# Optimization experiments

Measured on AMD Instinct MI355X. Metric: run time of the kernel, lower is better.

Reference implementation:

```python
import jax, jax.numpy as jnp
import numpy as np

NUM_GROUPS = 256   # number of distinct gt instance ids per image
EPS = 1e-6
PULL_W = 1.0
PUSH_W = 1.0
LOSS_W = 1.0


def setup_inputs() -> dict:
    key = jax.random.key(0)
    k1, k2, k3 = jax.random.split(key, 3)
    B, N, D = 16, 16384, 256
    pred = jax.random.normal(k1, (B, N, D), dtype=jnp.float32)
    gt_inds = jax.random.randint(k2, (B, N), 0, NUM_GROUPS, dtype=jnp.int32)
    anchor_inds = jax.random.randint(k3, (B, N), 0, 9, dtype=jnp.int32)
    return {"pred": pred, "gt_inds": gt_inds, "anchor_inds": anchor_inds}


def _single_image_loss(p, g):
    # p: [N, D] tag embeddings, g: [N] int group ids in [0, NUM_GROUPS)
    ones = jnp.ones(g.shape, dtype=p.dtype)
    counts = jax.ops.segment_sum(ones, g, num_segments=NUM_GROUPS)          # [G]
    sums = jax.ops.segment_sum(p, g, num_segments=NUM_GROUPS)               # [G, D]
    tags = sums / jnp.maximum(counts, 1.0)[:, None]                         # group means

    # pull: per-element cosine to own group's tag (torch cos eps clamp on norm product)
    tag_per = tags[g]                                                       # [N, D]
    dot = jnp.sum(p * tag_per, axis=1)
    denom = jnp.maximum(jnp.linalg.norm(p, axis=1) * jnp.linalg.norm(tag_per, axis=1), EPS)
    one_minus_cos = 1.0 - dot / denom                                       # [N]
    pull_g = jax.ops.segment_sum(one_minus_cos, g, num_segments=NUM_GROUPS) / jnp.maximum(counts, 1.0)

    present = counts > 0
    obj_num = jnp.sum(present.astype(p.dtype))
    pull = jnp.sum(jnp.where(present, pull_g, 0.0)) / (obj_num + EPS)

    # push: pairwise cosine over group tags (incl. diagonal, then subtract 2*obj_num)
    tn = jnp.linalg.norm(tags, axis=1)                                      # [G]
    cosmat = (tags @ tags.T) / jnp.maximum(tn[:, None] * tn[None, :], EPS)  # [G, G]
    pair_mask = present[:, None] & present[None, :]
    push_sum = jnp.sum(jnp.where(pair_mask, 1.0 + cosmat, 0.0)) - 2.0 * obj_num
    push = push_sum / (((obj_num - 1.0) * obj_num + EPS) * 2.0)

    loss = PUSH_W * push + PULL_W * pull
    # original returns 0 when only a single group exists
    return jnp.where(obj_num > 1.0, loss, 0.0)


def reference(pred, gt_inds, anchor_inds):
    per_img = jax.vmap(_single_image_loss)(pred, gt_inds)   # [B]
    return LOSS_W * jnp.mean(per_img)
```

## Files before the change

### kernel.cpp

```cpp
#include <hip/hip_runtime.h>

#define B_ 16
#define N_ 16384
#define D_ 256
#define G_ 256
#define EPSF 1e-6f
#define CHUNKS 16
#define CROWS (N_/CHUNKS)

template <int CTRL>
__device__ __forceinline__ float dpp_add_step(float x) {
    const int y = __builtin_amdgcn_update_dpp(0, __float_as_int(x), CTRL, 0xF, 0xF, false);
    return x + __int_as_float(y);
}
__device__ __forceinline__ float wave_sum64(float x) {
    x = dpp_add_step<0x111>(x);
    x = dpp_add_step<0x112>(x);
    x = dpp_add_step<0x114>(x);
    x = dpp_add_step<0x118>(x);
    x = dpp_add_step<0x142>(x);
    x = dpp_add_step<0x143>(x);
    return __int_as_float(__builtin_amdgcn_readlane(__float_as_int(x), 63));
}

__global__ __launch_bounds__(256) void k_hist(const int* __restrict__ gt,
                                              int* __restrict__ chist,
                                              int* __restrict__ done) {
    __shared__ int h[G_];
    const int tid = threadIdx.x, blk = blockIdx.x;
    if (blk == 0 && tid == 0) done[0] = 0;
    h[tid] = 0;
    __syncthreads();
    const int4 g4 = *(const int4*)&gt[blk*CROWS + tid*4];
    atomicAdd(&h[g4.x], 1);
    atomicAdd(&h[g4.y], 1);
    atomicAdd(&h[g4.z], 1);
    atomicAdd(&h[g4.w], 1);
    __syncthreads();
    chist[blk*G_ + tid] = h[tid];
}

__global__ __launch_bounds__(256) void k_scatscan(const int* __restrict__ gt,
                                                  const int* __restrict__ chist,
                                                  int* __restrict__ counts,
                                                  int* __restrict__ starts,
                                                  int* __restrict__ sorted) {
    __shared__ int scn[G_];
    __shared__ int cur[G_];
    const int g = threadIdx.x, blk = blockIdx.x;
    const int b = blk >> 4, chunk = blk & 15;

    int tot = 0, pre = 0;
    #pragma unroll
    for (int cc = 0; cc < CHUNKS; ++cc) {
        const int v = chist[((b<<4) + cc)*G_ + g];
        pre += (cc < chunk) ? v : 0;
        tot += v;
    }
    scn[g] = tot;
    __syncthreads();
    for (int off = 1; off < G_; off <<= 1) {
        const int v2 = (g >= off) ? scn[g - off] : 0;
        __syncthreads();
        scn[g] += v2;
        __syncthreads();
    }
    const int st = scn[g] - tot;
    if (chunk == 0) { counts[b*G_ + g] = tot; starts[b*G_ + g] = st; }
    cur[g] = st + pre;
    __syncthreads();

    const int rbase = chunk * CROWS;
    const int4 g4 = *(const int4*)&gt[b*N_ + rbase + g*4];
    const int r = rbase + g*4;
    int* sb = sorted + b*N_;
    sb[atomicAdd(&cur[g4.x], 1)] = r;
    sb[atomicAdd(&cur[g4.y], 1)] = r + 1;
    sb[atomicAdd(&cur[g4.z], 1)] = r + 2;
    sb[atomicAdd(&cur[g4.w], 1)] = r + 3;
}

__global__ __launch_bounds__(256, 5) void k_fused(const float* __restrict__ pred,
                                                  const int* __restrict__ sorted,
                                                  const int* __restrict__ starts,
                                                  const int* __restrict__ counts,
                                                  float* __restrict__ sums,
                                                  float* __restrict__ pull_g) {
    __shared__ float comb[2][2][2][D_];
    const int tid = threadIdx.x, lane = tid & 63, w = tid >> 6;
    const int sub = w >> 1, h = w & 1;
    const int gi = (blockIdx.x << 1) | sub;
    const int b = gi >> 8;
    const int start = starts[gi], cnt = counts[gi];
    const int c = lane * 4;

    const float* predb = pred + (size_t)b*N_*D_;
    const int*   sortb = sorted + b*N_ + start;

    float4 acc  = make_float4(0.f,0.f,0.f,0.f);
    float4 uacc = make_float4(0.f,0.f,0.f,0.f);

    const int half = (cnt + 1) >> 1;
    const int lo = h * half;
    const int hi = min(cnt, lo + half);
    int i = lo;

    if (cnt > 0 && cnt <= 128) {
        const int ids0 = sortb[min(lane, cnt-1)];
        int ids1 = 0;
        if (cnt > 64) ids1 = sortb[min(64 + lane, cnt-1)];
        #define GET2(k) (((k) < 64) ? __builtin_amdgcn_readlane(ids0, (k)) \
                                    : __builtin_amdgcn_readlane(ids1, (k) - 64))
        for (; i + 8 <= hi; i += 8) {
            const int r0 = GET2(i+0), r1 = GET2(i+1), r2 = GET2(i+2), r3 = GET2(i+3);
            const int r4 = GET2(i+4), r5 = GET2(i+5), r6 = GET2(i+6), r7 = GET2(i+7);
            const float4 p0 = *(const float4*)&predb[(size_t)r0*D_ + c];
            const float4 p1 = *(const float4*)&predb[(size_t)r1*D_ + c];
            const float4 p2 = *(const float4*)&predb[(size_t)r2*D_ + c];
            const float4 p3 = *(const float4*)&predb[(size_t)r3*D_ + c];
            const float4 p4 = *(const float4*)&predb[(size_t)r4*D_ + c];
            const float4 p5 = *(const float4*)&predb[(size_t)r5*D_ + c];
            const float4 p6 = *(const float4*)&predb[(size_t)r6*D_ + c];
            const float4 p7 = *(const float4*)&predb[(size_t)r7*D_ + c];
            float n0 = p0.x*p0.x + p0.y*p0.y + p0.z*p0.z + p0.w*p0.w;
            float n1 = p1.x*p1.x + p1.y*p1.y + p1.z*p1.z + p1.w*p1.w;
            float n2 = p2.x*p2.x + p2.y*p2.y + p2.z*p2.z + p2.w*p2.w;
            float n3 = p3.x*p3.x + p3.y*p3.y + p3.z*p3.z + p3.w*p3.w;
            float n4 = p4.x*p4.x + p4.y*p4.y + p4.z*p4.z + p4.w*p4.w;
            float n5 = p5.x*p5.x + p5.y*p5.y + p5.z*p5.z + p5.w*p5.w;
            float n6 = p6.x*p6.x + p6.y*p6.y + p6.z*p6.z + p6.w*p6.w;
            float n7 = p7.x*p7.x + p7.y*p7.y + p7.z*p7.z + p7.w*p7.w;
            n0 = wave_sum64(n0); n1 = wave_sum64(n1);
            n2 = wave_sum64(n2); n3 = wave_sum64(n3);
            n4 = wave_sum64(n4); n5 = wave_sum64(n5);
            n6 = wave_sum64(n6); n7 = wave_sum64(n7);
            const float q0 = __frsqrt_rn(n0), q1 = __frsqrt_rn(n1);
            const float q2 = __frsqrt_rn(n2), q3 = __frsqrt_rn(n3);
            const float q4 = __frsqrt_rn(n4), q5 = __frsqrt_rn(n5);
            const float q6 = __frsqrt_rn(n6), q7 = __frsqrt_rn(n7);
            acc.x  += ((p0.x + p1.x) + (p2.x + p3.x)) + ((p4.x + p5.x) + (p6.x + p7.x));
            acc.y  += ((p0.y + p1.y) + (p2.y + p3.y)) + ((p4.y + p5.y) + (p6.y + p7.y));
            acc.z  += ((p0.z + p1.z) + (p2.z + p3.z)) + ((p4.z + p5.z) + (p6.z + p7.z));
            acc.w  += ((p0.w + p1.w) + (p2.w + p3.w)) + ((p4.w + p5.w) + (p6.w + p7.w));
            uacc.x += ((p0.x*q0 + p1.x*q1) + (p2.x*q2 + p3.x*q3)) + ((p4.x*q4 + p5.x*q5) + (p6.x*q6 + p7.x*q7));
            uacc.y += ((p0.y*q0 + p1.y*q1) + (p2.y*q2 + p3.y*q3)) + ((p4.y*q4 + p5.y*q5) + (p6.y*q6 + p7.y*q7));
            uacc.z += ((p0.z*q0 + p1.z*q1) + (p2.z*q2 + p3.z*q3)) + ((p4.z*q4 + p5.z*q5) + (p6.z*q6 + p7.z*q7));
            uacc.w += ((p0.w*q0 + p1.w*q1) + (p2.w*q2 + p3.w*q3)) + ((p4.w*q4 + p5.w*q5) + (p6.w*q6 + p7.w*q7));
        }
        for (; i < hi; ++i) {
            const int r0 = GET2(i);
            const float4 p0 = *(const float4*)&predb[(size_t)r0*D_ + c];
            const float n0 = wave_sum64(p0.x*p0.x + p0.y*p0.y + p0.z*p0.z + p0.w*p0.w);
            const float q0 = __frsqrt_rn(n0);
            acc.x  += p0.x;    acc.y  += p0.y;    acc.z  += p0.z;    acc.w  += p0.w;
            uacc.x += p0.x*q0; uacc.y += p0.y*q0; uacc.z += p0.z*q0; uacc.w += p0.w*q0;
        }
        #undef GET2
    } else if (cnt > 128) {
        for (; i < hi; ++i) {
            const int r0 = sortb[i];
            const float4 p0 = *(const float4*)&predb[(size_t)r0*D_ + c];
            const float n0 = wave_sum64(p0.x*p0.x + p0.y*p0.y + p0.z*p0.z + p0.w*p0.w);
            const float q0 = __frsqrt_rn(n0);
            acc.x  += p0.x;    acc.y  += p0.y;    acc.z  += p0.z;    acc.w  += p0.w;
            uacc.x += p0.x*q0; uacc.y += p0.y*q0; uacc.z += p0.z*q0; uacc.w += p0.w*q0;
        }
    }

    *(float4*)&comb[sub][h][0][c] = acc;
    *(float4*)&comb[sub][h][1][c] = uacc;
    __syncthreads();
    if (h != 0) return;

    const float4 a2 = *(const float4*)&comb[sub][1][0][c];
    const float4 u2 = *(const float4*)&comb[sub][1][1][c];
    acc.x  += a2.x;  acc.y  += a2.y;  acc.z  += a2.z;  acc.w  += a2.w;
    uacc.x += u2.x;  uacc.y += u2.y;  uacc.z += u2.z;  uacc.w += u2.w;

    *(float4*)&sums[(size_t)gi*D_ + c] = acc;
    if (cnt == 0) {
        if (lane == 0) pull_g[gi] = 0.f;
        return;
    }
    const float ssq = wave_sum64(acc.x*acc.x + acc.y*acc.y + acc.z*acc.z + acc.w*acc.w);
    const float dus = wave_sum64(uacc.x*acc.x + uacc.y*acc.y + uacc.z*acc.z + uacc.w*acc.w);
    if (lane == 0) pull_g[gi] = (float)cnt - dus / sqrtf(ssq);
}

__global__ __launch_bounds__(256) void k_tags(const float* __restrict__ sums,
                                              const int* __restrict__ counts,
                                              const float* __restrict__ pull_g,
                                              float* __restrict__ lossv,
                                              int* __restrict__ done,
                                              float* __restrict__ out) {
    const int b = blockIdx.x;
    const int tid = threadIdx.x;
    const int lane = tid & 63;
    const int wave = tid >> 6;
    __shared__ float s_acc[D_];
    __shared__ float redA[256];
    __shared__ float redB[256];

    for (int i = tid; i < D_; i += 256) s_acc[i] = 0.f;
    __syncthreads();

    const int c = lane * 4;
    float4 sl = make_float4(0.f, 0.f, 0.f, 0.f);
    for (int g = wave; g < G_; g += 4) {
        const int cnt = counts[b*G_ + g];
        const float inv = 1.0f / fmaxf((float)cnt, 1.0f);
        const float4 sm = *(const float4*)&sums[((size_t)(b*G_ + g))*D_ + c];
        const float tx = sm.x*inv, tyv = sm.y*inv, tz = sm.z*inv, tw = sm.w*inv;
        const float sq = wave_sum64(tx*tx + tyv*tyv + tz*tz + tw*tw);
        if (cnt > 0) {
            const float it = __frsqrt_rn(sq);
            sl.x += tx*it; sl.y += tyv*it; sl.z += tz*it; sl.w += tw*it;
        }
    }
    atomicAdd(&s_acc[c+0], sl.x);
    atomicAdd(&s_acc[c+1], sl.y);
    atomicAdd(&s_acc[c+2], sl.z);
    atomicAdd(&s_acc[c+3], sl.w);
    __syncthreads();

    const int cnt_t = counts[b*G_ + tid];
    const float v = s_acc[tid];
    redA[tid] = v * v;
    redB[tid] = (cnt_t > 0) ? 1.f : 0.f;
    __syncthreads();
    for (int s = 128; s > 0; s >>= 1) {
        if (tid < s) { redA[tid] += redA[tid + s]; redB[tid] += redB[tid + s]; }
        __syncthreads();
    }
    float ssq = 0.f, obj = 0.f;
    if (tid == 0) { ssq = redA[0]; obj = redB[0]; }
    __syncthreads();

    redA[tid] = (cnt_t > 0) ? pull_g[b*G_ + tid] / (float)cnt_t : 0.f;
    __syncthreads();
    for (int s = 128; s > 0; s >>= 1) {
        if (tid < s) redA[tid] += redA[tid + s];
        __syncthreads();
    }
    if (tid == 0) {
        const float push = (obj*obj - 2.f*obj + ssq) / (((obj - 1.f)*obj + EPSF) * 2.f);
        const float pull = redA[0] / (obj + EPSF);
        const float loss = (obj > 1.f) ? (push + pull) : 0.f;
        __hip_atomic_store(&lossv[b], loss, __ATOMIC_RELEASE, __HIP_MEMORY_SCOPE_AGENT);
        const int o = __hip_atomic_fetch_add(&done[0], 1, __ATOMIC_ACQ_REL,
                                             __HIP_MEMORY_SCOPE_AGENT);
        if (o == B_ - 1) {
            float t = 0.f;
            #pragma unroll
            for (int bb = 0; bb < B_; ++bb)
                t += __hip_atomic_load(&lossv[bb], __ATOMIC_RELAXED, __HIP_MEMORY_SCOPE_AGENT);
            out[0] = t * (1.0f / (float)B_);
        }
    }
}

extern "C" void kernel_launch(void* const* d_in, const int* in_sizes, int n_in,
                              void* d_out, int out_size, void* d_ws, size_t ws_size,
                              hipStream_t stream) {
    const float* pred = (const float*)d_in[0];
    const int*   gt   = (const int*)d_in[1];
    float* out = (float*)d_out;

    char* ws = (char*)d_ws;
    const size_t SZ_SUMS = (size_t)B_*G_*D_*sizeof(float);
    const size_t SZ_I    = (size_t)B_*G_*sizeof(int);

    float* sums    = (float*)ws;                               ws += SZ_SUMS;
    int*   counts  = (int*)ws;                                 ws += SZ_I;
    int*   starts  = (int*)ws;                                 ws += SZ_I;
    float* pull_g  = (float*)ws;                               ws += SZ_I;
    float* lossv   = (float*)ws;                               ws += 64*sizeof(float);
    int*   done    = (int*)ws;                                 ws += 64*sizeof(int);
    int*   sorted  = (int*)ws;                                 ws += (size_t)B_*N_*sizeof(int);
    int*   chist   = (int*)ws;

    k_hist     <<<B_*CHUNKS, 256, 0, stream>>>(gt, chist, done);
    k_scatscan <<<B_*CHUNKS, 256, 0, stream>>>(gt, chist, counts, starts, sorted);
    k_fused    <<<B_*G_/2,   256, 0, stream>>>(pred, sorted, starts, counts, sums, pull_g);
    k_tags     <<<B_,        256, 0, stream>>>(sums, counts, pull_g, lossv, done, out);
}
```

Baseline: 85.44 us.

## Map one wave per group and unroll gather loop by sixteen with masking

Each wave now handles a whole group instead of two waves splitting a group and combining through shared memory with a block barrier. The grid shrinks to four groups per block. The small-group path becomes a 16-way unrolled loop with clamped indices and zero weights for the tail, so more loads are in flight per wave. Empty groups exit early. In exchange each wave carries twice the serial work, the tail iterations issue redundant loads, and the heavier register use comes with a lower occupancy hint.

```diff
diff --git a/kernel.cpp b/kernel.cpp
--- a/kernel.cpp
+++ b/kernel.cpp
@@ -80,84 +80,61 @@
     sb[atomicAdd(&cur[g4.w], 1)] = r + 3;
 }
 
-__global__ __launch_bounds__(256, 5) void k_fused(const float* __restrict__ pred,
+__global__ __launch_bounds__(256, 4) void k_fused(const float* __restrict__ pred,
                                                   const int* __restrict__ sorted,
                                                   const int* __restrict__ starts,
                                                   const int* __restrict__ counts,
                                                   float* __restrict__ sums,
                                                   float* __restrict__ pull_g) {
-    __shared__ float comb[2][2][2][D_];
     const int tid = threadIdx.x, lane = tid & 63, w = tid >> 6;
-    const int sub = w >> 1, h = w & 1;
-    const int gi = (blockIdx.x << 1) | sub;
+    const int gi = (blockIdx.x << 2) | w;
     const int b = gi >> 8;
     const int start = starts[gi], cnt = counts[gi];
     const int c = lane * 4;
 
+    if (cnt == 0) {
+        float4 z = make_float4(0.f,0.f,0.f,0.f);
+        *(float4*)&sums[(size_t)gi*D_ + c] = z;
+        if (lane == 0) pull_g[gi] = 0.f;
+        return;
+    }
+
     const float* predb = pred + (size_t)b*N_*D_;
     const int*   sortb = sorted + b*N_ + start;
 
     float4 acc  = make_float4(0.f,0.f,0.f,0.f);
     float4 uacc = make_float4(0.f,0.f,0.f,0.f);
 
-    const int half = (cnt + 1) >> 1;
-    const int lo = h * half;
-    const int hi = min(cnt, lo + half);
-    int i = lo;
-
-    if (cnt > 0 && cnt <= 128) {
+    if (cnt <= 128) {
         const int ids0 = sortb[min(lane, cnt-1)];
         int ids1 = 0;
         if (cnt > 64) ids1 = sortb[min(64 + lane, cnt-1)];
-        #define GET2(k) (((k) < 64) ? __builtin_amdgcn_readlane(ids0, (k)) \
-                                    : __builtin_amdgcn_readlane(ids1, (k) - 64))
-        for (; i + 8 <= hi; i += 8) {
-            const int r0 = GET2(i+0), r1 = GET2(i+1), r2 = GET2(i+2), r3 = GET2(i+3);
-            const int r4 = GET2(i+4), r5 = GET2(i+5), r6 = GET2(i+6), r7 = GET2(i+7);
-            const float4 p0 = *(const float4*)&predb[(size_t)r0*D_ + c];
-            const float4 p1 = *(const float4*)&predb[(size_t)r1*D_ + c];
-            const float4 p2 = *(const float4*)&predb[(size_t)r2*D_ + c];
-            const float4 p3 = *(const float4*)&predb[(size_t)r3*D_ + c];
-            const float4 p4 = *(const float4*)&predb[(size_t)r4*D_ + c];
-            const float4 p5 = *(const float4*)&predb[(size_t)r5*D_ + c];
-            const float4 p6 = *(const float4*)&predb[(size_t)r6*D_ + c];
-            const float4 p7 = *(const float4*)&predb[(size_t)r7*D_ + c];
-            float n0 = p0.x*p0.x + p0.y*p0.y + p0.z*p0.z + p0.w*p0.w;
-            float n1 = p1.x*p1.x + p1.y*p1.y + p1.z*p1.z + p1.w*p1.w;
-            float n2 = p2.x*p2.x + p2.y*p2.y + p2.z*p2.z + p2.w*p2.w;
-            float n3 = p3.x*p3.x + p3.y*p3.y + p3.z*p3.z + p3.w*p3.w;
-            float n4 = p4.x*p4.x + p4.y*p4.y + p4.z*p4.z + p4.w*p4.w;
-            float n5 = p5.x*p5.x + p5.y*p5.y + p5.z*p5.z + p5.w*p5.w;
-            float n6 = p6.x*p6.x + p6.y*p6.y + p6.z*p6.z + p6.w*p6.w;
-            float n7 = p7.x*p7.x + p7.y*p7.y + p7.z*p7.z + p7.w*p7.w;
-            n0 = wave_sum64(n0); n1 = wave_sum64(n1);
-            n2 = wave_sum64(n2); n3 = wave_sum64(n3);
-            n4 = wave_sum64(n4); n5 = wave_sum64(n5);
-            n6 = wave_sum64(n6); n7 = wave_sum64(n7);
-            const float q0 = __frsqrt_rn(n0), q1 = __frsqrt_rn(n1);
-            const float q2 = __frsqrt_rn(n2), q3 = __frsqrt_rn(n3);
-            const float q4 = __frsqrt_rn(n4), q5 = __frsqrt_rn(n5);
-            const float q6 = __frsqrt_rn(n6), q7 = __frsqrt_rn(n7);
-            acc.x  += ((p0.x + p1.x) + (p2.x + p3.x)) + ((p4.x + p5.x) + (p6.x + p7.x));
-            acc.y  += ((p0.y + p1.y) + (p2.y + p3.y)) + ((p4.y + p5.y) + (p6.y + p7.y));
-            acc.z  += ((p0.z + p1.z) + (p2.z + p3.z)) + ((p4.z + p5.z) + (p6.z + p7.z));
-            acc.w  += ((p0.w + p1.w) + (p2.w + p3.w)) + ((p4.w + p5.w) + (p6.w + p7.w));
-            uacc.x += ((p0.x*q0 + p1.x*q1) + (p2.x*q2 + p3.x*q3)) + ((p4.x*q4 + p5.x*q5) + (p6.x*q6 + p7.x*q7));
-            uacc.y += ((p0.y*q0 + p1.y*q1) + (p2.y*q2 + p3.y*q3)) + ((p4.y*q4 + p5.y*q5) + (p6.y*q6 + p7.y*q7));
-            uacc.z += ((p0.z*q0 + p1.z*q1) + (p2.z*q2 + p3.z*q3)) + ((p4.z*q4 + p5.z*q5) + (p6.z*q6 + p7.z*q7));
-            uacc.w += ((p0.w*q0 + p1.w*q1) + (p2.w*q2 + p3.w*q3)) + ((p4.w*q4 + p5.w*q5) + (p6.w*q6 + p7.w*q7));
-        }
-        for (; i < hi; ++i) {
-            const int r0 = GET2(i);
-            const float4 p0 = *(const float4*)&predb[(size_t)r0*D_ + c];
-            const float n0 = wave_sum64(p0.x*p0.x + p0.y*p0.y + p0.z*p0.z + p0.w*p0.w);
-            const float q0 = __frsqrt_rn(n0);
-            acc.x  += p0.x;    acc.y  += p0.y;    acc.z  += p0.z;    acc.w  += p0.w;
-            uacc.x += p0.x*q0; uacc.y += p0.y*q0; uacc.z += p0.z*q0; uacc.w += p0.w*q0;
-        }
-        #undef GET2
-    } else if (cnt > 128) {
-        for (; i < hi; ++i) {
+
+        for (int i = 0; i < cnt; i += 16) {
+            float4 p[16];
+            float  wt[16];
+            #pragma unroll
+            for (int u = 0; u < 16; ++u) {
+                const int k  = i + u;
+                const int kk = min(k, cnt - 1);
+                const int r  = (kk < 64) ? __builtin_amdgcn_readlane(ids0, kk)
+                                         : __builtin_amdgcn_readlane(ids1, kk - 64);
+                p[u]  = *(const float4*)&predb[(size_t)r*D_ + c];
+                wt[u] = (k < cnt) ? 1.f : 0.f;
+            }
+            #pragma unroll
+            for (int u = 0; u < 16; ++u) {
+                float n = p[u].x*p[u].x + p[u].y*p[u].y + p[u].z*p[u].z + p[u].w*p[u].w;
+                n = wave_sum64(n);
+                const float q = __frsqrt_rn(n) * wt[u];
+                acc.x  += p[u].x * wt[u];  acc.y  += p[u].y * wt[u];
+                acc.z  += p[u].z * wt[u];  acc.w  += p[u].w * wt[u];
+                uacc.x += p[u].x * q;      uacc.y += p[u].y * q;
+                uacc.z += p[u].z * q;      uacc.w += p[u].w * q;
+            }
+        }
+    } else {
+        for (int i = 0; i < cnt; ++i) {
             const int r0 = sortb[i];
             const float4 p0 = *(const float4*)&predb[(size_t)r0*D_ + c];
             const float n0 = wave_sum64(p0.x*p0.x + p0.y*p0.y + p0.z*p0.z + p0.w*p0.w);
@@ -167,21 +144,7 @@
         }
     }
 
-    *(float4*)&comb[sub][h][0][c] = acc;
-    *(float4*)&comb[sub][h][1][c] = uacc;
-    __syncthreads();
-    if (h != 0) return;
-
-    const float4 a2 = *(const float4*)&comb[sub][1][0][c];
-    const float4 u2 = *(const float4*)&comb[sub][1][1][c];
-    acc.x  += a2.x;  acc.y  += a2.y;  acc.z  += a2.z;  acc.w  += a2.w;
-    uacc.x += u2.x;  uacc.y += u2.y;  uacc.z += u2.z;  uacc.w += u2.w;
-
     *(float4*)&sums[(size_t)gi*D_ + c] = acc;
-    if (cnt == 0) {
-        if (lane == 0) pull_g[gi] = 0.f;
-        return;
-    }
     const float ssq = wave_sum64(acc.x*acc.x + acc.y*acc.y + acc.z*acc.z + acc.w*acc.w);
     const float dus = wave_sum64(uacc.x*acc.x + uacc.y*acc.y + uacc.z*acc.z + uacc.w*acc.w);
     if (lane == 0) pull_g[gi] = (float)cnt - dus / sqrtf(ssq);
@@ -281,6 +244,6 @@
 
     k_hist     <<<B_*CHUNKS, 256, 0, stream>>>(gt, chist, done);
     k_scatscan <<<B_*CHUNKS, 256, 0, stream>>>(gt, chist, counts, starts, sorted);
-    k_fused    <<<B_*G_/2,   256, 0, stream>>>(pred, sorted, starts, counts, sums, pull_g);
+    k_fused    <<<B_*G_/4,   256, 0, stream>>>(pred, sorted, starts, counts, sums, pull_g);
     k_tags     <<<B_,        256, 0, stream>>>(sums, counts, pull_g, lossv, done, out);
 }
```

Measured after the change: 85.83 us. No clear change (+0.5%).
